# Optimization experiments

Measured on AMD Instinct MI355X. Metric: run time of the kernel, lower is better.

Reference implementation:

```python
import jax, jax.numpy as jnp
import numpy as np

B = 64          # molecules per batch
N_ATOMS = 16    # atoms per molecule (uniform -> torch.split == reshape)
DIM = 128
N = B * N_ATOMS # 1024 total atoms
N_FP = 10000
N_BOND_FP = 10000
EPS = 1e-12     # F.normalize default eps


def setup_inputs() -> dict:
    key = jax.random.key(0)
    ks = jax.random.split(key, 12)
    s = 1.0 / np.sqrt(DIM)
    # block-diagonal structure: molecule id per atom
    mol = jnp.arange(N) // N_ATOMS
    block = mol[:, None] == mol[None, :]
    fingerprints = jax.random.randint(ks[0], (N,), 0, N_FP, dtype=jnp.int32)
    # pad() fills off-block with 0.0; in-block: sparse binary bonds
    adjacency = jnp.where(block, (jax.random.uniform(ks[1], (N, N)) < 0.3).astype(jnp.float32), 0.0)
    # pad_MPO() fills off-block with index 0 (which still embeds to a real row!)
    bond_index = jnp.where(block, jax.random.randint(ks[2], (N, N), 0, N_BOND_FP, dtype=jnp.int32), 0)
    return {
        "fingerprints": fingerprints,
        "adjacency": adjacency,
        "bond_index": bond_index,
        "E_fp": jax.random.normal(ks[3], (N_FP, DIM), jnp.float32),
        "E_bond": jax.random.normal(ks[4], (N_BOND_FP, DIM), jnp.float32),
        "W_fp": jax.random.normal(ks[5], (DIM, DIM), jnp.float32) * s,
        "b_fp": jnp.zeros((DIM,), jnp.float32),
        "W_out0": jax.random.normal(ks[6], (DIM, DIM), jnp.float32) * s,
        "b_out0": jnp.zeros((DIM,), jnp.float32),
        "W_out1": jax.random.normal(ks[7], (DIM, DIM), jnp.float32) * s,
        "b_out1": jnp.zeros((DIM,), jnp.float32),
        "W_prop": jax.random.normal(ks[8], (DIM, 1), jnp.float32) * s,
        "b_prop": jnp.zeros((1,), jnp.float32),
    }


def _l2norm(x, axis):
    n = jnp.sqrt(jnp.sum(x * x, axis=axis, keepdims=True))
    return x / jnp.maximum(n, EPS)


def reference(fingerprints, adjacency, bond_index, E_fp, E_bond, W_fp, b_fp,
              W_out0, b_out0, W_out1, b_out1, W_prop, b_prop):
    # MPS: atom embeddings + one round of dense (block-diag) message passing
    mps = E_fp[fingerprints]                                   # [N, d]
    contri = jax.nn.relu(mps @ W_fp + b_fp)                    # [N, d]
    mps = mps + adjacency @ contri                             # [N, d]
    mps = _l2norm(mps, axis=1)                                 # F.normalize(., 2, 1)
    # MPO: embedding of the padded [N, N] bond index -> [N, N, d]
    mpo = E_bond[bond_index]                                   # [N, N, d]
    mpo = _l2norm(mpo, axis=1)                                 # normalize over 2nd atom axis
    # tmp[c, b] = sum_a mps[a, c] * mpo[a, b, c]
    tmp = jnp.einsum('ac,abc->cb', mps, mpo)                   # [d, N]
    # uniform molecular_sizes -> torch.split == reshape
    info = tmp.reshape(DIM, B, N_ATOMS)                        # [d, B, n]
    fv = mps.reshape(B, N_ATOMS, DIM)                          # [B, n, d]
    tn = jnp.einsum('dmn,mnd->md', info, fv)                   # [B, d]
    x = jax.nn.relu(tn @ W_out0 + b_out0)
    x = jax.nn.relu(x @ W_out1 + b_out1)
    return x @ W_prop + b_prop                                 # [B, 1]
```

## Files before the change

kernel.cpp:

```cpp
#include <hip/hip_runtime.h>
#include <math.h>

#define DIM_   128
#define NAT_   16
#define NTOT_  1024
#define BMOL_  64
#define OFFB_  1008.0f
#define EPSF_  1e-12f

__global__ __launch_bounds__(512) void kA(const int* __restrict__ fp,
                                          const float* __restrict__ Efp,
                                          const float* __restrict__ Wfp,
                                          const float* __restrict__ bfp,
                                          const float* __restrict__ adj,
                                          const int* __restrict__ bidx,
                                          const float* __restrict__ Ebond,
                                          float* __restrict__ TnIn_g,
                                          float* __restrict__ Mb_g,
                                          float* __restrict__ Sb_g) {
    const int m = blockIdx.x, base = m * NAT_;
    const int t = threadIdx.x;
    const int c = t & 127;
    const int s = t >> 7;

    __shared__ float mpsS[NAT_][DIM_];
    __shared__ float conS[NAT_][DIM_];
    __shared__ float adjS[NAT_][NAT_];
    __shared__ int   bSh[NAT_][NAT_];
    __shared__ float redS[NAT_][2];
    __shared__ float nrmS[NAT_];
    __shared__ float red4[4][NAT_][DIM_];
    __shared__ float sb4[4][DIM_];
    __shared__ float tnp[4][DIM_];

    #pragma unroll
    for (int r = 0; r < 4; ++r) {
        const int idx = t + r * 512;
        const int j = idx >> 7, cc = idx & 127;
        mpsS[j][cc] = Efp[(size_t)fp[base + j] * DIM_ + cc];
    }
    if (t < 256) {
        const int j = t >> 4, i = t & 15;
        adjS[j][i] = adj[(size_t)(base + j) * NTOT_ + base + i];
        bSh[j][i]  = bidx[(size_t)(base + j) * NTOT_ + base + i];
    }
    __syncthreads();

    float acc[4];
    const float bb = bfp[c];
    #pragma unroll
    for (int jj = 0; jj < 4; ++jj) acc[jj] = bb;
    for (int k = 0; k < DIM_; ++k) {
        const float w = Wfp[k * DIM_ + c];
        #pragma unroll
        for (int jj = 0; jj < 4; ++jj) acc[jj] += mpsS[s * 4 + jj][k] * w;
    }
    #pragma unroll
    for (int jj = 0; jj < 4; ++jj) conS[s * 4 + jj][c] = fmaxf(acc[jj], 0.0f);
    __syncthreads();

    float ms[4];
    #pragma unroll
    for (int jj = 0; jj < 4; ++jj) {
        const int j = s * 4 + jj;
        float a = mpsS[j][c];
        #pragma unroll
        for (int i = 0; i < NAT_; ++i) a += adjS[j][i] * conS[i][c];
        ms[jj] = a;
    }
    const int half = c >> 6;
    #pragma unroll
    for (int jj = 0; jj < 4; ++jj) {
        const int j = s * 4 + jj;
        float v = ms[jj] * ms[jj];
        for (int o = 32; o > 0; o >>= 1) v += __shfl_xor(v, o, 64);
        if ((t & 63) == 0) redS[j][half] = v;
    }
    __syncthreads();
    if (t < NAT_) nrmS[t] = fmaxf(sqrtf(redS[t][0] + redS[t][1]), EPSF_);
    __syncthreads();

    float mn[4];
    #pragma unroll
    for (int jj = 0; jj < 4; ++jj) {
        const int j = s * 4 + jj;
        mn[jj] = ms[jj] / nrmS[j];
        mpsS[j][c] = mn[jj];
    }

    const float e0 = Ebond[c];
    const float e0sq = OFFB_ * e0 * e0;
    float accIn[NAT_];
    #pragma unroll
    for (int i = 0; i < NAT_; ++i) accIn[i] = 0.0f;
    float sb = 0.0f;
    #pragma unroll
    for (int jj = 0; jj < 4; ++jj) {
        const int j = s * 4 + jj;
        float ev[NAT_];
        #pragma unroll
        for (int i = 0; i < NAT_; ++i)
            ev[i] = Ebond[(size_t)bSh[j][i] * DIM_ + c];
        float nsq = e0sq;
        #pragma unroll
        for (int i = 0; i < NAT_; ++i) nsq += ev[i] * ev[i];
        const float mscj = mn[jj] / fmaxf(sqrtf(nsq), EPSF_);
        sb += mscj;
        #pragma unroll
        for (int i = 0; i < NAT_; ++i) accIn[i] += mscj * ev[i];
    }
    #pragma unroll
    for (int i = 0; i < NAT_; ++i) red4[s][i][c] = accIn[i];
    sb4[s][c] = sb;
    __syncthreads();

    float tnpart = 0.0f;
    #pragma unroll
    for (int ii = 0; ii < 4; ++ii) {
        const int i = s * 4 + ii;
        const float in_i = red4[0][i][c] + red4[1][i][c] + red4[2][i][c] + red4[3][i][c];
        tnpart += in_i * mpsS[i][c];
    }
    tnp[s][c] = tnpart;
    __syncthreads();

    if (s == 0) {
        const float TnIn = tnp[0][c] + tnp[1][c] + tnp[2][c] + tnp[3][c];
        const float Sb   = sb4[0][c] + sb4[1][c] + sb4[2][c] + sb4[3][c];
        float Mb = 0.0f;
        #pragma unroll
        for (int j = 0; j < NAT_; ++j) Mb += mpsS[j][c];
        TnIn_g[m * DIM_ + c] = TnIn;
        Sb_g[m * DIM_ + c]   = Sb;
        Mb_g[m * DIM_ + c]   = Mb;
    }
}

__global__ __launch_bounds__(128) void kB(const float* __restrict__ Ebond,
                                          const float* __restrict__ TnIn_g,
                                          const float* __restrict__ Mb_g,
                                          const float* __restrict__ Sb_g,
                                          const float* __restrict__ W0, const float* __restrict__ b0,
                                          const float* __restrict__ W1, const float* __restrict__ b1,
                                          const float* __restrict__ Wp, const float* __restrict__ bp,
                                          float* __restrict__ out) {
    const int m = blockIdx.x, c = threadIdx.x;
    __shared__ float tnS[DIM_];
    __shared__ float r2[2];

    float S = 0.0f;
    #pragma unroll 8
    for (int mm = 0; mm < BMOL_; ++mm) S += Sb_g[mm * DIM_ + c];
    const float tn = TnIn_g[m * DIM_ + c]
                   + Ebond[c] * (S - Sb_g[m * DIM_ + c]) * Mb_g[m * DIM_ + c];
    tnS[c] = tn;
    __syncthreads();

    float x0 = b0[c];
    #pragma unroll 8
    for (int d = 0; d < DIM_; ++d) x0 += tnS[d] * W0[d * DIM_ + c];
    x0 = fmaxf(x0, 0.0f);
    __syncthreads();
    tnS[c] = x0;
    __syncthreads();
    float x1 = b1[c];
    #pragma unroll 8
    for (int d = 0; d < DIM_; ++d) x1 += tnS[d] * W1[d * DIM_ + c];
    x1 = fmaxf(x1, 0.0f);

    float v = x1 * Wp[c];
    for (int o = 32; o > 0; o >>= 1) v += __shfl_xor(v, o, 64);
    if ((c & 63) == 0) r2[c >> 6] = v;
    __syncthreads();
    if (c == 0) out[m] = r2[0] + r2[1] + bp[0];
}

extern "C" void kernel_launch(void* const* d_in, const int* in_sizes, int n_in,
                              void* d_out, int out_size, void* d_ws, size_t ws_size,
                              hipStream_t stream) {
    const int*   fingerprints = (const int*)  d_in[0];
    const float* adjacency    = (const float*)d_in[1];
    const int*   bond_index   = (const int*)  d_in[2];
    const float* E_fp         = (const float*)d_in[3];
    const float* E_bond       = (const float*)d_in[4];
    const float* W_fp         = (const float*)d_in[5];
    const float* b_fp         = (const float*)d_in[6];
    const float* W_out0       = (const float*)d_in[7];
    const float* b_out0       = (const float*)d_in[8];
    const float* W_out1       = (const float*)d_in[9];
    const float* b_out1       = (const float*)d_in[10];
    const float* W_prop       = (const float*)d_in[11];
    const float* b_prop       = (const float*)d_in[12];
    float* out = (float*)d_out;

    float* ws = (float*)d_ws;
    const size_t MD = (size_t)BMOL_ * DIM_;
    float* TnIn = ws;
    float* Mb   = ws + MD;
    float* Sb   = ws + 2 * MD;

    kA<<<BMOL_, 512, 0, stream>>>(fingerprints, E_fp, W_fp, b_fp, adjacency, bond_index,
                                  E_bond, TnIn, Mb, Sb);
    kB<<<BMOL_, DIM_, 0, stream>>>(E_bond, TnIn, Mb, Sb,
                                   W_out0, b_out0, W_out1, b_out1, W_prop, b_prop, out);
}
```

Baseline: 22.98 us.

## Double kA block size to 1024 threads, two atoms per thread

Kernel A now runs 1024 threads per molecule block, so each thread handles two atom rows instead of four. The per-thread serial work (matvec, gather of bond embeddings, accumulation) halves. The cross-group reduction in shared memory is restructured into a two-phase add with an extra barrier. Only 64 blocks launch, so more threads per block is meant to expose more parallelism and latency hiding on a mostly idle GPU, at the cost of more register pressure and synchronisation.

```diff
diff --git a/kernel.cpp b/kernel.cpp
--- a/kernel.cpp
+++ b/kernel.cpp
@@ -8,20 +8,21 @@
 #define OFFB_  1008.0f
 #define EPSF_  1e-12f
 
-__global__ __launch_bounds__(512) void kA(const int* __restrict__ fp,
-                                          const float* __restrict__ Efp,
-                                          const float* __restrict__ Wfp,
-                                          const float* __restrict__ bfp,
-                                          const float* __restrict__ adj,
-                                          const int* __restrict__ bidx,
-                                          const float* __restrict__ Ebond,
-                                          float* __restrict__ TnIn_g,
-                                          float* __restrict__ Mb_g,
-                                          float* __restrict__ Sb_g) {
+__global__ __launch_bounds__(1024) void kA(const int* __restrict__ fp,
+                                           const float* __restrict__ Efp,
+                                           const float* __restrict__ Wfp,
+                                           const float* __restrict__ bfp,
+                                           const float* __restrict__ adj,
+                                           const int* __restrict__ bidx,
+                                           const float* __restrict__ Ebond,
+                                           float* __restrict__ TnIn_g,
+                                           float* __restrict__ Mb_g,
+                                           float* __restrict__ Sb_g) {
     const int m = blockIdx.x, base = m * NAT_;
     const int t = threadIdx.x;
     const int c = t & 127;
     const int s = t >> 7;
+    const int j0 = 2 * s, j1 = 2 * s + 1;
 
     __shared__ float mpsS[NAT_][DIM_];
     __shared__ float conS[NAT_][DIM_];
@@ -30,104 +31,110 @@
     __shared__ float redS[NAT_][2];
     __shared__ float nrmS[NAT_];
     __shared__ float red4[4][NAT_][DIM_];
-    __shared__ float sb4[4][DIM_];
-    __shared__ float tnp[4][DIM_];
-
-    #pragma unroll
-    for (int r = 0; r < 4; ++r) {
-        const int idx = t + r * 512;
-        const int j = idx >> 7, cc = idx & 127;
+    __shared__ float sb8[8][DIM_];
+    __shared__ float tnp8[8][DIM_];
+
+    {
+        int j = t >> 7, cc = t & 127;
+        mpsS[j][cc] = Efp[(size_t)fp[base + j] * DIM_ + cc];
+        j += 8;
         mpsS[j][cc] = Efp[(size_t)fp[base + j] * DIM_ + cc];
     }
     if (t < 256) {
         const int j = t >> 4, i = t & 15;
         adjS[j][i] = adj[(size_t)(base + j) * NTOT_ + base + i];
-        bSh[j][i]  = bidx[(size_t)(base + j) * NTOT_ + base + i];
-    }
-    __syncthreads();
-
-    float acc[4];
-    const float bb = bfp[c];
-    #pragma unroll
-    for (int jj = 0; jj < 4; ++jj) acc[jj] = bb;
+    } else if (t < 512) {
+        const int tt = t - 256, j = tt >> 4, i = tt & 15;
+        bSh[j][i] = bidx[(size_t)(base + j) * NTOT_ + base + i];
+    }
+    __syncthreads();
+
+    float a0 = bfp[c];
+    float a1 = a0;
+    #pragma unroll 8
     for (int k = 0; k < DIM_; ++k) {
-        const float w = Wfp[k * DIM_ + c];
-        #pragma unroll
-        for (int jj = 0; jj < 4; ++jj) acc[jj] += mpsS[s * 4 + jj][k] * w;
-    }
-    #pragma unroll
-    for (int jj = 0; jj < 4; ++jj) conS[s * 4 + jj][c] = fmaxf(acc[jj], 0.0f);
-    __syncthreads();
-
-    float ms[4];
-    #pragma unroll
-    for (int jj = 0; jj < 4; ++jj) {
-        const int j = s * 4 + jj;
-        float a = mpsS[j][c];
-        #pragma unroll
-        for (int i = 0; i < NAT_; ++i) a += adjS[j][i] * conS[i][c];
-        ms[jj] = a;
-    }
-    const int half = c >> 6;
-    #pragma unroll
-    for (int jj = 0; jj < 4; ++jj) {
-        const int j = s * 4 + jj;
-        float v = ms[jj] * ms[jj];
-        for (int o = 32; o > 0; o >>= 1) v += __shfl_xor(v, o, 64);
-        if ((t & 63) == 0) redS[j][half] = v;
-    }
+        const float w = Wfp[(size_t)k * DIM_ + c];
+        a0 += mpsS[j0][k] * w;
+        a1 += mpsS[j1][k] * w;
+    }
+    conS[j0][c] = fmaxf(a0, 0.0f);
+    conS[j1][c] = fmaxf(a1, 0.0f);
+    __syncthreads();
+
+    float ms0 = mpsS[j0][c], ms1 = mpsS[j1][c];
+    #pragma unroll
+    for (int i = 0; i < NAT_; ++i) {
+        const float cv = conS[i][c];
+        ms0 += adjS[j0][i] * cv;
+        ms1 += adjS[j1][i] * cv;
+    }
+    float v0 = ms0 * ms0, v1 = ms1 * ms1;
+    #pragma unroll
+    for (int o = 32; o > 0; o >>= 1) {
+        v0 += __shfl_xor(v0, o, 64);
+        v1 += __shfl_xor(v1, o, 64);
+    }
+    const int half = (t >> 6) & 1;
+    if ((t & 63) == 0) { redS[j0][half] = v0; redS[j1][half] = v1; }
     __syncthreads();
     if (t < NAT_) nrmS[t] = fmaxf(sqrtf(redS[t][0] + redS[t][1]), EPSF_);
     __syncthreads();
 
-    float mn[4];
-    #pragma unroll
-    for (int jj = 0; jj < 4; ++jj) {
-        const int j = s * 4 + jj;
-        mn[jj] = ms[jj] / nrmS[j];
-        mpsS[j][c] = mn[jj];
-    }
+    const float mn0 = ms0 / nrmS[j0];
+    const float mn1 = ms1 / nrmS[j1];
+    mpsS[j0][c] = mn0;
+    mpsS[j1][c] = mn1;
 
     const float e0 = Ebond[c];
     const float e0sq = OFFB_ * e0 * e0;
+    float evA[NAT_], evB[NAT_];
+    #pragma unroll
+    for (int i = 0; i < NAT_; ++i)
+        evA[i] = Ebond[(size_t)bSh[j0][i] * DIM_ + c];
+    #pragma unroll
+    for (int i = 0; i < NAT_; ++i)
+        evB[i] = Ebond[(size_t)bSh[j1][i] * DIM_ + c];
+    float nsqA = e0sq, nsqB = e0sq;
+    #pragma unroll
+    for (int i = 0; i < NAT_; ++i) {
+        nsqA += evA[i] * evA[i];
+        nsqB += evB[i] * evB[i];
+    }
+    const float mscA = mn0 / fmaxf(sqrtf(nsqA), EPSF_);
+    const float mscB = mn1 / fmaxf(sqrtf(nsqB), EPSF_);
     float accIn[NAT_];
     #pragma unroll
-    for (int i = 0; i < NAT_; ++i) accIn[i] = 0.0f;
-    float sb = 0.0f;
-    #pragma unroll
-    for (int jj = 0; jj < 4; ++jj) {
-        const int j = s * 4 + jj;
-        float ev[NAT_];
-        #pragma unroll
-        for (int i = 0; i < NAT_; ++i)
-            ev[i] = Ebond[(size_t)bSh[j][i] * DIM_ + c];
-        float nsq = e0sq;
-        #pragma unroll
-        for (int i = 0; i < NAT_; ++i) nsq += ev[i] * ev[i];
-        const float mscj = mn[jj] / fmaxf(sqrtf(nsq), EPSF_);
-        sb += mscj;
-        #pragma unroll
-        for (int i = 0; i < NAT_; ++i) accIn[i] += mscj * ev[i];
-    }
-    #pragma unroll
-    for (int i = 0; i < NAT_; ++i) red4[s][i][c] = accIn[i];
-    sb4[s][c] = sb;
-    __syncthreads();
-
-    float tnpart = 0.0f;
-    #pragma unroll
-    for (int ii = 0; ii < 4; ++ii) {
-        const int i = s * 4 + ii;
-        const float in_i = red4[0][i][c] + red4[1][i][c] + red4[2][i][c] + red4[3][i][c];
-        tnpart += in_i * mpsS[i][c];
-    }
-    tnp[s][c] = tnpart;
+    for (int i = 0; i < NAT_; ++i)
+        accIn[i] = mscA * evA[i] + mscB * evB[i];
+
+    if (s < 4) {
+        #pragma unroll
+        for (int i = 0; i < NAT_; ++i) red4[s][i][c] = accIn[i];
+    }
+    sb8[s][c] = mscA + mscB;
+    __syncthreads();
+    if (s >= 4) {
+        #pragma unroll
+        for (int i = 0; i < NAT_; ++i) red4[s - 4][i][c] += accIn[i];
+    }
+    __syncthreads();
+
+    float in0 = 0.0f, in1 = 0.0f;
+    #pragma unroll
+    for (int s2 = 0; s2 < 4; ++s2) {
+        in0 += red4[s2][j0][c];
+        in1 += red4[s2][j1][c];
+    }
+    tnp8[s][c] = in0 * mn0 + in1 * mn1;
     __syncthreads();
 
     if (s == 0) {
-        const float TnIn = tnp[0][c] + tnp[1][c] + tnp[2][c] + tnp[3][c];
-        const float Sb   = sb4[0][c] + sb4[1][c] + sb4[2][c] + sb4[3][c];
-        float Mb = 0.0f;
+        float TnIn = 0.0f, Sb = 0.0f, Mb = 0.0f;
+        #pragma unroll
+        for (int s2 = 0; s2 < 8; ++s2) {
+            TnIn += tnp8[s2][c];
+            Sb   += sb8[s2][c];
+        }
         #pragma unroll
         for (int j = 0; j < NAT_; ++j) Mb += mpsS[j][c];
         TnIn_g[m * DIM_ + c] = TnIn;
@@ -158,17 +165,18 @@
 
     float x0 = b0[c];
     #pragma unroll 8
-    for (int d = 0; d < DIM_; ++d) x0 += tnS[d] * W0[d * DIM_ + c];
+    for (int d = 0; d < DIM_; ++d) x0 += tnS[d] * W0[(size_t)d * DIM_ + c];
     x0 = fmaxf(x0, 0.0f);
     __syncthreads();
     tnS[c] = x0;
     __syncthreads();
     float x1 = b1[c];
     #pragma unroll 8
-    for (int d = 0; d < DIM_; ++d) x1 += tnS[d] * W1[d * DIM_ + c];
+    for (int d = 0; d < DIM_; ++d) x1 += tnS[d] * W1[(size_t)d * DIM_ + c];
     x1 = fmaxf(x1, 0.0f);
 
     float v = x1 * Wp[c];
+    #pragma unroll
     for (int o = 32; o > 0; o >>= 1) v += __shfl_xor(v, o, 64);
     if ((c & 63) == 0) r2[c >> 6] = v;
     __syncthreads();
@@ -199,8 +207,8 @@
     float* Mb   = ws + MD;
     float* Sb   = ws + 2 * MD;
 
-    kA<<<BMOL_, 512, 0, stream>>>(fingerprints, E_fp, W_fp, b_fp, adjacency, bond_index,
-                                  E_bond, TnIn, Mb, Sb);
+    kA<<<BMOL_, 1024, 0, stream>>>(fingerprints, E_fp, W_fp, b_fp, adjacency, bond_index,
+                                   E_bond, TnIn, Mb, Sb);
     kB<<<BMOL_, DIM_, 0, stream>>>(E_bond, TnIn, Mb, Sb,
                                    W_out0, b_out0, W_out1, b_out1, W_prop, b_prop, out);
 }
```

Measured after the change: 23.48 us. 2.2% more time.

## Fuse both kernels with a grid barrier and split each molecule across four blocks

Applied to the files above, without the earlier changes.

The two kernels become one launch of 256 blocks, four per molecule. Each block recomputes the molecule's message-passing step and handles four rows of the bond gather. A global atomic counter acts as a grid barrier, after which one block per molecule reduces the partial sums and runs the MLP head. The W_fp matmul is also reorganised to split K across the waves. This removes a kernel launch and spreads the gather across more CUs. In exchange it adds a memset, a spin-wait that assumes all 256 blocks are co-resident, and redundant per-block recomputation of the embedding and message-passing work.

```diff
diff --git a/kernel.cpp b/kernel.cpp
--- a/kernel.cpp
+++ b/kernel.cpp
@@ -5,33 +5,40 @@
 #define NAT_   16
 #define NTOT_  1024
 #define BMOL_  64
+#define NBLK_  256
 #define OFFB_  1008.0f
 #define EPSF_  1e-12f
 
-__global__ __launch_bounds__(512) void kA(const int* __restrict__ fp,
-                                          const float* __restrict__ Efp,
-                                          const float* __restrict__ Wfp,
-                                          const float* __restrict__ bfp,
-                                          const float* __restrict__ adj,
-                                          const int* __restrict__ bidx,
-                                          const float* __restrict__ Ebond,
-                                          float* __restrict__ TnIn_g,
-                                          float* __restrict__ Mb_g,
-                                          float* __restrict__ Sb_g) {
-    const int m = blockIdx.x, base = m * NAT_;
+__global__ __launch_bounds__(512) void fused(
+    const int* __restrict__ fp, const float* __restrict__ Efp,
+    const float* __restrict__ Wfp, const float* __restrict__ bfp,
+    const float* __restrict__ adj, const int* __restrict__ bidx,
+    const float* __restrict__ Ebond,
+    const float* __restrict__ W0, const float* __restrict__ b0,
+    const float* __restrict__ W1, const float* __restrict__ b1,
+    const float* __restrict__ Wp, const float* __restrict__ bp,
+    float* __restrict__ SbP_g, float* __restrict__ TnP_g,
+    unsigned* __restrict__ bar, float* __restrict__ out)
+{
+    const int bid = blockIdx.x;
+    const int m = bid >> 2, sub = bid & 3, base = m * NAT_;
     const int t = threadIdx.x;
     const int c = t & 127;
     const int s = t >> 7;
 
     __shared__ float mpsS[NAT_][DIM_];
+    __shared__ float conP[4][NAT_][DIM_];
     __shared__ float conS[NAT_][DIM_];
     __shared__ float adjS[NAT_][NAT_];
-    __shared__ int   bSh[NAT_][NAT_];
-    __shared__ float redS[NAT_][2];
+    __shared__ int   bSh[4][NAT_];
+    __shared__ float nrmRed[NAT_][2];
     __shared__ float nrmS[NAT_];
-    __shared__ float red4[4][NAT_][DIM_];
+    __shared__ float w4[4][DIM_];
     __shared__ float sb4[4][DIM_];
-    __shared__ float tnp[4][DIM_];
+    __shared__ float mbS[DIM_];
+    __shared__ float vS[DIM_];
+    __shared__ float tnS[DIM_];
+    __shared__ float r2[2];
 
     #pragma unroll
     for (int r = 0; r < 4; ++r) {
@@ -42,137 +49,166 @@
     if (t < 256) {
         const int j = t >> 4, i = t & 15;
         adjS[j][i] = adj[(size_t)(base + j) * NTOT_ + base + i];
-        bSh[j][i]  = bidx[(size_t)(base + j) * NTOT_ + base + i];
-    }
-    __syncthreads();
-
-    float acc[4];
-    const float bb = bfp[c];
-    #pragma unroll
-    for (int jj = 0; jj < 4; ++jj) acc[jj] = bb;
-    for (int k = 0; k < DIM_; ++k) {
-        const float w = Wfp[k * DIM_ + c];
-        #pragma unroll
-        for (int jj = 0; jj < 4; ++jj) acc[jj] += mpsS[s * 4 + jj][k] * w;
-    }
-    #pragma unroll
-    for (int jj = 0; jj < 4; ++jj) conS[s * 4 + jj][c] = fmaxf(acc[jj], 0.0f);
-    __syncthreads();
-
-    float ms[4];
-    #pragma unroll
-    for (int jj = 0; jj < 4; ++jj) {
-        const int j = s * 4 + jj;
-        float a = mpsS[j][c];
-        #pragma unroll
-        for (int i = 0; i < NAT_; ++i) a += adjS[j][i] * conS[i][c];
-        ms[jj] = a;
-    }
-    const int half = c >> 6;
-    #pragma unroll
-    for (int jj = 0; jj < 4; ++jj) {
-        const int j = s * 4 + jj;
-        float v = ms[jj] * ms[jj];
+    } else if (t < 320) {
+        const int tt = t - 256, j = tt >> 4, i = tt & 15;
+        bSh[j][i] = bidx[(size_t)(base + 4 * sub + j) * NTOT_ + base + i];
+    }
+    __syncthreads();
+
+    {
+        float a[NAT_];
+        #pragma unroll
+        for (int j = 0; j < NAT_; ++j) a[j] = 0.0f;
+        #pragma unroll 4
+        for (int kk = 0; kk < 32; ++kk) {
+            const int k = (s << 5) + kk;
+            const float w = Wfp[(size_t)k * DIM_ + c];
+            #pragma unroll
+            for (int j = 0; j < NAT_; ++j) a[j] += mpsS[j][k] * w;
+        }
+        #pragma unroll
+        for (int j = 0; j < NAT_; ++j) conP[s][j][c] = a[j];
+    }
+    __syncthreads();
+    #pragma unroll
+    for (int r = 0; r < 4; ++r) {
+        const int idx = t + r * 512;
+        const int j = idx >> 7, cc = idx & 127;
+        conS[j][cc] = fmaxf(conP[0][j][cc] + conP[1][j][cc] + conP[2][j][cc]
+                          + conP[3][j][cc] + bfp[cc], 0.0f);
+    }
+    __syncthreads();
+
+    float msv[4];
+    #pragma unroll
+    for (int u = 0; u < 4; ++u) {
+        const int i = s + 4 * u;
+        float x = mpsS[i][c];
+        #pragma unroll
+        for (int q = 0; q < NAT_; ++q) x += adjS[i][q] * conS[q][c];
+        msv[u] = x;
+        float v = x * x;
+        #pragma unroll
         for (int o = 32; o > 0; o >>= 1) v += __shfl_xor(v, o, 64);
-        if ((t & 63) == 0) redS[j][half] = v;
-    }
-    __syncthreads();
-    if (t < NAT_) nrmS[t] = fmaxf(sqrtf(redS[t][0] + redS[t][1]), EPSF_);
-    __syncthreads();
-
-    float mn[4];
-    #pragma unroll
-    for (int jj = 0; jj < 4; ++jj) {
-        const int j = s * 4 + jj;
-        mn[jj] = ms[jj] / nrmS[j];
-        mpsS[j][c] = mn[jj];
-    }
-
-    const float e0 = Ebond[c];
-    const float e0sq = OFFB_ * e0 * e0;
-    float accIn[NAT_];
-    #pragma unroll
-    for (int i = 0; i < NAT_; ++i) accIn[i] = 0.0f;
-    float sb = 0.0f;
-    #pragma unroll
-    for (int jj = 0; jj < 4; ++jj) {
-        const int j = s * 4 + jj;
+        if ((t & 63) == 0) nrmRed[i][(t >> 6) & 1] = v;
+    }
+    __syncthreads();
+    if (t < NAT_) nrmS[t] = fmaxf(sqrtf(nrmRed[t][0] + nrmRed[t][1]), EPSF_);
+    __syncthreads();
+    #pragma unroll
+    for (int u = 0; u < 4; ++u) {
+        const int i = s + 4 * u;
+        mpsS[i][c] = msv[u] / nrmS[i];
+    }
+    __syncthreads();
+
+    {
+        const float e0 = Ebond[c];
+        float nsq = OFFB_ * e0 * e0;
         float ev[NAT_];
-        #pragma unroll
-        for (int i = 0; i < NAT_; ++i)
-            ev[i] = Ebond[(size_t)bSh[j][i] * DIM_ + c];
-        float nsq = e0sq;
+        int bb[NAT_];
+        #pragma unroll
+        for (int i = 0; i < NAT_; ++i) bb[i] = bSh[s][i];
+        #pragma unroll
+        for (int i = 0; i < NAT_; ++i) ev[i] = Ebond[(size_t)bb[i] * DIM_ + c];
         #pragma unroll
         for (int i = 0; i < NAT_; ++i) nsq += ev[i] * ev[i];
-        const float mscj = mn[jj] / fmaxf(sqrtf(nsq), EPSF_);
-        sb += mscj;
-        #pragma unroll
-        for (int i = 0; i < NAT_; ++i) accIn[i] += mscj * ev[i];
-    }
-    #pragma unroll
-    for (int i = 0; i < NAT_; ++i) red4[s][i][c] = accIn[i];
-    sb4[s][c] = sb;
-    __syncthreads();
-
-    float tnpart = 0.0f;
-    #pragma unroll
-    for (int ii = 0; ii < 4; ++ii) {
-        const int i = s * 4 + ii;
-        const float in_i = red4[0][i][c] + red4[1][i][c] + red4[2][i][c] + red4[3][i][c];
-        tnpart += in_i * mpsS[i][c];
-    }
-    tnp[s][c] = tnpart;
+        const float msc = mpsS[4 * sub + s][c] / fmaxf(sqrtf(nsq), EPSF_);
+        float tj = 0.0f;
+        #pragma unroll
+        for (int i = 0; i < NAT_; ++i) tj += ev[i] * mpsS[i][c];
+        w4[s][c]  = msc * tj;
+        sb4[s][c] = msc;
+    }
     __syncthreads();
 
     if (s == 0) {
-        const float TnIn = tnp[0][c] + tnp[1][c] + tnp[2][c] + tnp[3][c];
-        const float Sb   = sb4[0][c] + sb4[1][c] + sb4[2][c] + sb4[3][c];
-        float Mb = 0.0f;
-        #pragma unroll
-        for (int j = 0; j < NAT_; ++j) Mb += mpsS[j][c];
-        TnIn_g[m * DIM_ + c] = TnIn;
-        Sb_g[m * DIM_ + c]   = Sb;
-        Mb_g[m * DIM_ + c]   = Mb;
-    }
-}
-
-__global__ __launch_bounds__(128) void kB(const float* __restrict__ Ebond,
-                                          const float* __restrict__ TnIn_g,
-                                          const float* __restrict__ Mb_g,
-                                          const float* __restrict__ Sb_g,
-                                          const float* __restrict__ W0, const float* __restrict__ b0,
-                                          const float* __restrict__ W1, const float* __restrict__ b1,
-                                          const float* __restrict__ Wp, const float* __restrict__ bp,
-                                          float* __restrict__ out) {
-    const int m = blockIdx.x, c = threadIdx.x;
-    __shared__ float tnS[DIM_];
-    __shared__ float r2[2];
-
-    float S = 0.0f;
-    #pragma unroll 8
-    for (int mm = 0; mm < BMOL_; ++mm) S += Sb_g[mm * DIM_ + c];
-    const float tn = TnIn_g[m * DIM_ + c]
-                   + Ebond[c] * (S - Sb_g[m * DIM_ + c]) * Mb_g[m * DIM_ + c];
-    tnS[c] = tn;
-    __syncthreads();
-
-    float x0 = b0[c];
-    #pragma unroll 8
-    for (int d = 0; d < DIM_; ++d) x0 += tnS[d] * W0[d * DIM_ + c];
-    x0 = fmaxf(x0, 0.0f);
-    __syncthreads();
-    tnS[c] = x0;
-    __syncthreads();
-    float x1 = b1[c];
-    #pragma unroll 8
-    for (int d = 0; d < DIM_; ++d) x1 += tnS[d] * W1[d * DIM_ + c];
-    x1 = fmaxf(x1, 0.0f);
-
-    float v = x1 * Wp[c];
-    for (int o = 32; o > 0; o >>= 1) v += __shfl_xor(v, o, 64);
-    if ((c & 63) == 0) r2[c >> 6] = v;
-    __syncthreads();
-    if (c == 0) out[m] = r2[0] + r2[1] + bp[0];
+        const float TnP = w4[0][c] + w4[1][c] + w4[2][c] + w4[3][c];
+        const float SbP = sb4[0][c] + sb4[1][c] + sb4[2][c] + sb4[3][c];
+        __hip_atomic_store(&TnP_g[(size_t)bid * DIM_ + c], TnP, __ATOMIC_RELAXED, __HIP_MEMORY_SCOPE_AGENT);
+        __hip_atomic_store(&SbP_g[(size_t)bid * DIM_ + c], SbP, __ATOMIC_RELAXED, __HIP_MEMORY_SCOPE_AGENT);
+    }
+    if (sub == 0 && s == 1) {
+        float mb = 0.0f;
+        #pragma unroll
+        for (int i = 0; i < NAT_; ++i) mb += mpsS[i][c];
+        mbS[c] = mb;
+    }
+    __syncthreads();
+
+    if (t == 0) {
+        __threadfence();
+        __hip_atomic_fetch_add(bar, 1u, __ATOMIC_ACQ_REL, __HIP_MEMORY_SCOPE_AGENT);
+    }
+    if (sub != 0) return;
+    if (t == 0) {
+        unsigned cur;
+        do {
+            __builtin_amdgcn_s_sleep(2);
+            cur = __hip_atomic_load(bar, __ATOMIC_ACQUIRE, __HIP_MEMORY_SCOPE_AGENT);
+        } while (cur < (unsigned)NBLK_);
+    }
+    __syncthreads();
+
+    {
+        float S = 0.0f;
+        for (int rb = 0; rb < 4; ++rb) {
+            float tv[16];
+            #pragma unroll
+            for (int r = 0; r < 16; ++r)
+                tv[r] = __hip_atomic_load(&SbP_g[(size_t)(s * 64 + rb * 16 + r) * DIM_ + c],
+                                          __ATOMIC_RELAXED, __HIP_MEMORY_SCOPE_AGENT);
+            #pragma unroll
+            for (int r = 0; r < 16; ++r) S += tv[r];
+        }
+        w4[s][c] = S;
+    }
+    __syncthreads();
+    if (s == 0) {
+        const float Sall = w4[0][c] + w4[1][c] + w4[2][c] + w4[3][c];
+        float Sb_m = 0.0f, Tn_m = 0.0f;
+        #pragma unroll
+        for (int u = 0; u < 4; ++u) {
+            Sb_m += __hip_atomic_load(&SbP_g[(size_t)(4 * m + u) * DIM_ + c],
+                                      __ATOMIC_RELAXED, __HIP_MEMORY_SCOPE_AGENT);
+            Tn_m += __hip_atomic_load(&TnP_g[(size_t)(4 * m + u) * DIM_ + c],
+                                      __ATOMIC_RELAXED, __HIP_MEMORY_SCOPE_AGENT);
+        }
+        vS[c] = Tn_m + Ebond[c] * (Sall - Sb_m) * mbS[c];
+    }
+    __syncthreads();
+
+    {
+        float a1 = 0.0f;
+        #pragma unroll 8
+        for (int r = 0; r < 32; ++r) {
+            const int d = s * 32 + r;
+            a1 += vS[d] * W0[(size_t)d * DIM_ + c];
+        }
+        w4[s][c] = a1;
+    }
+    __syncthreads();
+    if (s == 0) tnS[c] = fmaxf(w4[0][c] + w4[1][c] + w4[2][c] + w4[3][c] + b0[c], 0.0f);
+    __syncthreads();
+    {
+        float a2 = 0.0f;
+        #pragma unroll 8
+        for (int r = 0; r < 32; ++r) {
+            const int d = s * 32 + r;
+            a2 += tnS[d] * W1[(size_t)d * DIM_ + c];
+        }
+        w4[s][c] = a2;
+    }
+    __syncthreads();
+    if (s == 0) {
+        const float x1 = fmaxf(w4[0][c] + w4[1][c] + w4[2][c] + w4[3][c] + b1[c], 0.0f);
+        float vv = x1 * Wp[c];
+        #pragma unroll
+        for (int o = 32; o > 0; o >>= 1) vv += __shfl_xor(vv, o, 64);
+        if ((c & 63) == 0) r2[c >> 6] = vv;
+    }
+    __syncthreads();
+    if (t == 0) out[m] = r2[0] + r2[1] + bp[0];
 }
 
 extern "C" void kernel_launch(void* const* d_in, const int* in_sizes, int n_in,
@@ -194,13 +230,14 @@
     float* out = (float*)d_out;
 
     float* ws = (float*)d_ws;
-    const size_t MD = (size_t)BMOL_ * DIM_;
-    float* TnIn = ws;
-    float* Mb   = ws + MD;
-    float* Sb   = ws + 2 * MD;
-
-    kA<<<BMOL_, 512, 0, stream>>>(fingerprints, E_fp, W_fp, b_fp, adjacency, bond_index,
-                                  E_bond, TnIn, Mb, Sb);
-    kB<<<BMOL_, DIM_, 0, stream>>>(E_bond, TnIn, Mb, Sb,
-                                   W_out0, b_out0, W_out1, b_out1, W_prop, b_prop, out);
+    const size_t PD = (size_t)NBLK_ * DIM_;
+    float* SbP = ws;
+    float* TnP = ws + PD;
+    unsigned* bar = (unsigned*)(ws + 2 * PD);
+
+    hipMemsetAsync(bar, 0, sizeof(unsigned), stream);
+    fused<<<NBLK_, 512, 0, stream>>>(fingerprints, E_fp, W_fp, b_fp,
+                                     adjacency, bond_index, E_bond,
+                                     W_out0, b_out0, W_out1, b_out1, W_prop, b_prop,
+                                     SbP, TnP, bar, out);
 }
```

Result: slower. 32.17 us (+40.0%).
